# Kernel tuning notes

Measured on AMD Instinct MI355X. Metric: run time of the kernel, lower is better.

Reference implementation:

```python
import jax, jax.numpy as jnp
import numpy as np

LENGTH = 4096
BATCH = 4096
N_OBS = 2


def setup_inputs() -> dict:
    key = jax.random.key(0)
    k1, k2, k3 = jax.random.split(key, 3)
    # Scale potentials down: the original chain performs no message
    # normalization, so we keep per-step log-growth tiny to avoid overflow.
    j = jax.random.normal(k1, (), dtype=jnp.float32) * 0.01
    b = jax.random.normal(k2, (N_OBS,), dtype=jnp.float32) * 0.01
    observations = jax.random.randint(k3, (BATCH, LENGTH), 0, N_OBS, dtype=jnp.int32)
    return {"j": j, "b": b, "observations": observations}


def reference(j, b, observations):
    # Max-product belief propagation on a binary-state chain CRF,
    # vectorized over the batch and scanned over the chain length.
    B, L = observations.shape
    values = jnp.array([-0.5, 0.5], dtype=jnp.float32)          # states {0,1} - 0.5
    pairs = values[:, None] * values[None, :]                    # [2,2] outer product
    psi = jnp.exp(j * pairs)                                     # [2,2] pairwise potential
    # Unary potentials phi[b_idx, i, s] = exp(b[obs] * values[s])
    phi = jnp.exp(b[observations][..., None] * values)           # [B,L,2]
    phi_tm = jnp.transpose(phi, (1, 0, 2))                       # time-major [L,B,2]

    def step(msg, phi_t):
        # msg_new[k] = max_l phi_t[l] * msg[l] * psi[k,l]
        x = phi_t * msg                                          # [B,2]
        new = jnp.max(x[:, None, :] * psi[None, :, :], axis=2)   # [B,2]
        return new, new

    ones = jnp.ones((B, 2), dtype=phi.dtype)
    # Forward messages: column 0 is ones, column t uses obs[0..t-1]
    _, fwd_msgs = jax.lax.scan(step, ones, phi_tm[:-1])          # [L-1,B,2]
    forward = jnp.concatenate([ones[None], fwd_msgs], axis=0)    # [L,B,2]
    # Backward messages: iterate i = L-1 .. 1, last column is ones
    _, bwd_msgs = jax.lax.scan(step, ones, phi_tm[1:][::-1])     # [L-1,B,2]
    backward = jnp.concatenate([bwd_msgs[::-1], ones[None]], axis=0)  # [L,B,2]

    beliefs = phi_tm * forward * backward                        # [L,B,2]
    return jnp.transpose(beliefs, (1, 2, 0))                     # [B,2,L]
```

## Files before the change

kernel.cpp:

```cpp
#include <hip/hip_runtime.h>
#include <hip/hip_bf16.h>
#include <math.h>

#define LENGTH 4096
#define BATCH  4096
#define CHUNK  16
#define NTHR   256

__device__ __forceinline__ void mp_compose(
    float a00, float a01, float a10, float a11,
    float b00, float b01, float b10, float b11,
    float& d00, float& d01, float& d10, float& d11) {
  d00 = fmaxf(a00 + b00, a01 + b10);
  d01 = fmaxf(a00 + b01, a01 + b11);
  d10 = fmaxf(a10 + b00, a11 + b10);
  d11 = fmaxf(a10 + b01, a11 + b11);
}

__global__ __launch_bounds__(NTHR, 4) void chain_bp_kernel(
    const float* __restrict__ jp, const float* __restrict__ bp,
    const int* __restrict__ obs, float* __restrict__ out) {
  const int row  = blockIdx.x;
  const int tid  = threadIdx.x;
  const int lane = tid & 63;
  const int wv   = tid >> 6;

  const float j  = jp[0];
  const float q  = 0.25f * j;
  const float u0 = 0.5f * bp[0];
  const float u1 = 0.5f * bp[1];
  const float wb = -fabsf(q);

  const int t0 = tid * CHUNK;
  const int4* op = reinterpret_cast<const int4*>(obs + (size_t)row * LENGTH + t0);
  float u[CHUNK];
#pragma unroll
  for (int v = 0; v < CHUNK / 4; ++v) {
    int4 o = op[v];
    u[4 * v + 0] = o.x ? u1 : u0;
    u[4 * v + 1] = o.y ? u1 : u0;
    u[4 * v + 2] = o.z ? u1 : u0;
    u[4 * v + 3] = o.w ? u1 : u0;
  }

  float f00 = -u[0] + q, f01 = u[0] - q, f10 = -u[0] - q, f11 = u[0] + q;
#pragma unroll
  for (int i = 1; i < CHUNK; ++i) {
    float ui = u[i];
    float a0l0 = f00 - ui, a1l0 = f10 + ui;
    float a0l1 = f01 - ui, a1l1 = f11 + ui;
    float n00 = fmaxf(a0l0 + q, a1l0 - q);
    float n10 = fmaxf(a0l0 - q, a1l0 + q);
    float n01 = fmaxf(a0l1 + q, a1l1 - q);
    float n11 = fmaxf(a0l1 - q, a1l1 + q);
    f00 = n00; f01 = n01; f10 = n10; f11 = n11;
  }

  float x00 = f00, x01 = f01, x10 = f10, x11 = f11;
#pragma unroll
  for (int d = 1; d < 64; d <<= 1) {
    float p00 = __shfl_up(x00, d), p01 = __shfl_up(x01, d);
    float p10 = __shfl_up(x10, d), p11 = __shfl_up(x11, d);
    if (lane >= d) {
      float n00, n01, n10, n11;
      mp_compose(x00, x01, x10, x11, p00, p01, p10, p11, n00, n01, n10, n11);
      x00 = n00; x01 = n01; x10 = n10; x11 = n11;
    }
  }
  float y00 = f00, y01 = f10, y10 = f01, y11 = f11;
#pragma unroll
  for (int d = 1; d < 64; d <<= 1) {
    float p00 = __shfl_down(y00, d), p01 = __shfl_down(y01, d);
    float p10 = __shfl_down(y10, d), p11 = __shfl_down(y11, d);
    if (lane + d < 64) {
      float n00, n01, n10, n11;
      mp_compose(y00, y01, y10, y11, p00, p01, p10, p11, n00, n01, n10, n11);
      y00 = n00; y01 = n01; y10 = n10; y11 = n11;
    }
  }

  __shared__ float smp[4][4];
  __shared__ float sms[4][4];
  if (lane == 63) { smp[wv][0] = x00; smp[wv][1] = x01; smp[wv][2] = x10; smp[wv][3] = x11; }
  if (lane == 0)  { sms[wv][0] = y00; sms[wv][1] = y01; sms[wv][2] = y10; sms[wv][3] = y11; }
  __syncthreads();

  float fh0 = 0.f, fh1 = 0.f;
  for (int k = 0; k < wv; ++k) {
    float m00 = smp[k][0], m01 = smp[k][1], m10 = smp[k][2], m11 = smp[k][3];
    float n0 = fmaxf(m00 + fh0, m01 + fh1);
    float n1 = fmaxf(m10 + fh0, m11 + fh1);
    fh0 = n0; fh1 = n1;
  }
  float wt0 = wb, wt1 = wb;
  for (int k = 3; k > wv; --k) {
    float m00 = sms[k][0], m01 = sms[k][1], m10 = sms[k][2], m11 = sms[k][3];
    float n0 = fmaxf(m00 + wt0, m01 + wt1);
    float n1 = fmaxf(m10 + wt0, m11 + wt1);
    wt0 = n0; wt1 = n1;
  }

  float z0 = fmaxf(x00 + fh0, x01 + fh1);
  float z1 = fmaxf(x10 + fh0, x11 + fh1);
  float zp0 = __shfl_up(z0, 1), zp1 = __shfl_up(z1, 1);
  float fi0 = (lane == 0) ? fh0 : zp0;
  float fi1 = (lane == 0) ? fh1 : zp1;

  float yv0 = fmaxf(y00 + wt0, y01 + wt1);
  float yv1 = fmaxf(y10 + wt0, y11 + wt1);
  float yn0 = __shfl_down(yv0, 1), yn1 = __shfl_down(yv1, 1);
  float wc0 = (lane == 63) ? wt0 : yn0;
  float wc1 = (lane == 63) ? wt1 : yn1;
  float g0 = fmaxf(q + wc0, -q + wc1);
  float g1 = fmaxf(-q + wc0, q + wc1);

  float b0[CHUNK], b1[CHUNK];
  b0[CHUNK - 1] = g0; b1[CHUNK - 1] = g1;
#pragma unroll
  for (int i = CHUNK - 1; i > 0; --i) {
    float ui = u[i];
    float a0 = b0[i] - ui;
    float a1 = b1[i] + ui;
    b0[i - 1] = fmaxf(a0 + q, a1 - q);
    b1[i - 1] = fmaxf(a0 - q, a1 + q);
  }

  float* outp = out + (size_t)row * (2 * LENGTH) + t0;
  float fw0 = fi0, fw1 = fi1;
  float4 acc0, acc1;
#pragma unroll
  for (int i = 0; i < CHUNK; ++i) {
    float ui = u[i];
    float e0 = __expf(-ui + fw0 + b0[i]);
    float e1 = __expf( ui + fw1 + b1[i]);
    (&acc0.x)[i & 3] = e0;
    (&acc1.x)[i & 3] = e1;
    if ((i & 3) == 3) {
      *reinterpret_cast<float4*>(outp + (i - 3))          = acc0;
      *reinterpret_cast<float4*>(outp + LENGTH + (i - 3)) = acc1;
    }
    float a0 = fw0 - ui, a1 = fw1 + ui;
    float n0 = fmaxf(a0 + q, a1 - q);
    float n1 = fmaxf(a0 - q, a1 + q);
    fw0 = n0; fw1 = n1;
  }
}

extern "C" void kernel_launch(void* const* d_in, const int* in_sizes, int n_in,
                              void* d_out, int out_size, void* d_ws, size_t ws_size,
                              hipStream_t stream) {
  const float* jp  = (const float*)d_in[0];
  const float* bp  = (const float*)d_in[1];
  const int*   obs = (const int*)d_in[2];
  float* out = (float*)d_out;

  chain_bp_kernel<<<BATCH, NTHR, 0, stream>>>(jp, bp, obs, out);
}
```

Baseline: 200.7 us.

## Halve per-thread chunk, double block threads, split local scan, nontemporal stores

```diff
diff --git a/kernel.cpp b/kernel.cpp
--- a/kernel.cpp
+++ b/kernel.cpp
@@ -4,8 +4,11 @@
 
 #define LENGTH 4096
 #define BATCH  4096
-#define CHUNK  16
-#define NTHR   256
+#define CHUNK  8
+#define NTHR   512
+#define NWAVE  (NTHR / 64)
+
+typedef float vf4 __attribute__((ext_vector_type(4)));
 
 __device__ __forceinline__ void mp_compose(
     float a00, float a01, float a10, float a11,
@@ -17,7 +20,18 @@
   d11 = fmaxf(a10 + b01, a11 + b11);
 }
 
-__global__ __launch_bounds__(NTHR, 4) void chain_bp_kernel(
+__device__ __forceinline__ void mp_step(
+    float& f00, float& f01, float& f10, float& f11, float ui, float q) {
+  float a0l0 = f00 - ui, a1l0 = f10 + ui;
+  float a0l1 = f01 - ui, a1l1 = f11 + ui;
+  float n00 = fmaxf(a0l0 + q, a1l0 - q);
+  float n10 = fmaxf(a0l0 - q, a1l0 + q);
+  float n01 = fmaxf(a0l1 + q, a1l1 - q);
+  float n11 = fmaxf(a0l1 - q, a1l1 + q);
+  f00 = n00; f01 = n01; f10 = n10; f11 = n11;
+}
+
+__global__ __launch_bounds__(NTHR, 6) void chain_bp_kernel(
     const float* __restrict__ jp, const float* __restrict__ bp,
     const int* __restrict__ obs, float* __restrict__ out) {
   const int row  = blockIdx.x;
@@ -43,18 +57,15 @@
     u[4 * v + 3] = o.w ? u1 : u0;
   }
 
-  float f00 = -u[0] + q, f01 = u[0] - q, f10 = -u[0] - q, f11 = u[0] + q;
+  float l00 = -u[0] + q, l01 = u[0] - q, l10 = -u[0] - q, l11 = u[0] + q;
+  float h00 = -u[4] + q, h01 = u[4] - q, h10 = -u[4] - q, h11 = u[4] + q;
 #pragma unroll
-  for (int i = 1; i < CHUNK; ++i) {
-    float ui = u[i];
-    float a0l0 = f00 - ui, a1l0 = f10 + ui;
-    float a0l1 = f01 - ui, a1l1 = f11 + ui;
-    float n00 = fmaxf(a0l0 + q, a1l0 - q);
-    float n10 = fmaxf(a0l0 - q, a1l0 + q);
-    float n01 = fmaxf(a0l1 + q, a1l1 - q);
-    float n11 = fmaxf(a0l1 - q, a1l1 + q);
-    f00 = n00; f01 = n01; f10 = n10; f11 = n11;
+  for (int i = 1; i < 4; ++i) {
+    mp_step(l00, l01, l10, l11, u[i], q);
+    mp_step(h00, h01, h10, h11, u[4 + i], q);
   }
+  float f00, f01, f10, f11;
+  mp_compose(h00, h01, h10, h11, l00, l01, l10, l11, f00, f01, f10, f11);
 
   float x00 = f00, x01 = f01, x10 = f10, x11 = f11;
 #pragma unroll
@@ -79,8 +90,8 @@
     }
   }
 
-  __shared__ float smp[4][4];
-  __shared__ float sms[4][4];
+  __shared__ float smp[NWAVE][4];
+  __shared__ float sms[NWAVE][4];
   if (lane == 63) { smp[wv][0] = x00; smp[wv][1] = x01; smp[wv][2] = x10; smp[wv][3] = x11; }
   if (lane == 0)  { sms[wv][0] = y00; sms[wv][1] = y01; sms[wv][2] = y10; sms[wv][3] = y11; }
   __syncthreads();
@@ -93,7 +104,7 @@
     fh0 = n0; fh1 = n1;
   }
   float wt0 = wb, wt1 = wb;
-  for (int k = 3; k > wv; --k) {
+  for (int k = NWAVE - 1; k > wv; --k) {
     float m00 = sms[k][0], m01 = sms[k][1], m10 = sms[k][2], m11 = sms[k][3];
     float n0 = fmaxf(m00 + wt0, m01 + wt1);
     float n1 = fmaxf(m10 + wt0, m11 + wt1);
@@ -127,17 +138,17 @@
 
   float* outp = out + (size_t)row * (2 * LENGTH) + t0;
   float fw0 = fi0, fw1 = fi1;
-  float4 acc0, acc1;
+  vf4 acc0, acc1;
 #pragma unroll
   for (int i = 0; i < CHUNK; ++i) {
     float ui = u[i];
     float e0 = __expf(-ui + fw0 + b0[i]);
     float e1 = __expf( ui + fw1 + b1[i]);
-    (&acc0.x)[i & 3] = e0;
-    (&acc1.x)[i & 3] = e1;
+    acc0[i & 3] = e0;
+    acc1[i & 3] = e1;
     if ((i & 3) == 3) {
-      *reinterpret_cast<float4*>(outp + (i - 3))          = acc0;
-      *reinterpret_cast<float4*>(outp + LENGTH + (i - 3)) = acc1;
+      __builtin_nontemporal_store(acc0, reinterpret_cast<vf4*>(outp + (i - 3)));
+      __builtin_nontemporal_store(acc1, reinterpret_cast<vf4*>(outp + LENGTH + (i - 3)));
     }
     float a0 = fw0 - ui, a1 = fw1 + ui;
     float n0 = fmaxf(a0 + q, a1 - q);
```

After: 223.1 us. 11.2% more time.
